# Kernel optimization log

Hardware: AMD Instinct MI355X
Metric: run time of the kernel (lower is better)

## Reference

```python
import jax, jax.numpy as jnp
import numpy as np

N, P, C, H, W, M = 2, 3, 80, 64, 64, 524288
HID = 64
BOX_WARP = 2.0


def _linear_init(key, fan_in, fan_out):
    # kaiming-uniform-ish; bias is zero-init per the torch module
    bound = 1.0 / np.sqrt(fan_in)
    return jax.random.uniform(key, (fan_in, fan_out), jnp.float32, -bound, bound)


def setup_inputs() -> dict:
    key = jax.random.key(0)
    ks = jax.random.split(key, 6)
    planes = jax.random.normal(ks[0], (N, P, C, H, W), jnp.float32)
    coordinates = jax.random.uniform(ks[1], (N, M, 3), jnp.float32, -1.0, 1.0)
    W1 = _linear_init(ks[2], 3 * C, HID)
    W2 = _linear_init(ks[3], HID, HID)
    W3 = _linear_init(ks[4], HID, HID)
    W4 = _linear_init(ks[5], HID, 1)
    return {
        "planes": planes, "coordinates": coordinates,
        "W1": W1, "b1": jnp.zeros((HID,), jnp.float32),
        "W2": W2, "b2": jnp.zeros((HID,), jnp.float32),
        "W3": W3, "b3": jnp.zeros((HID,), jnp.float32),
        "W4": W4, "b4": jnp.zeros((1,), jnp.float32),
    }


def _grid_sample_bilinear(feat, grid):
    # feat: [B, C, H, W]; grid: [B, M, 2] in [-1, 1] (x, y order),
    # bilinear, padding_mode='zeros', align_corners=False (matches torch).
    B, Cc, Hh, Ww = feat.shape
    gx = (grid[..., 0] + 1.0) * (Ww * 0.5) - 0.5  # [B, M]
    gy = (grid[..., 1] + 1.0) * (Hh * 0.5) - 0.5
    x0 = jnp.floor(gx)
    y0 = jnp.floor(gy)
    wx1 = gx - x0
    wy1 = gy - y0
    featf = feat.transpose(0, 2, 3, 1).reshape(B, Hh * Ww, Cc)  # [B, HW, C]

    def gather(xi, yi):
        valid = (xi >= 0) & (xi < Ww) & (yi >= 0) & (yi < Hh)
        xc = jnp.clip(xi, 0, Ww - 1).astype(jnp.int32)
        yc = jnp.clip(yi, 0, Hh - 1).astype(jnp.int32)
        idx = yc * Ww + xc  # [B, M]
        v = jnp.take_along_axis(featf, idx[..., None], axis=1)  # [B, M, C]
        return v * valid[..., None].astype(feat.dtype)

    v00 = gather(x0, y0)
    v01 = gather(x0 + 1, y0)
    v10 = gather(x0, y0 + 1)
    v11 = gather(x0 + 1, y0 + 1)
    wx1 = wx1[..., None]
    wy1 = wy1[..., None]
    top = v00 * (1.0 - wx1) + v01 * wx1
    bot = v10 * (1.0 - wx1) + v11 * wx1
    return top * (1.0 - wy1) + bot * wy1  # [B, M, C]


def _plane_axes():
    return jnp.array(
        [[[1, 0, 0], [0, 1, 0], [0, 0, 1]],
         [[1, 0, 0], [0, 0, 1], [0, 1, 0]],
         [[0, 0, 1], [0, 1, 0], [1, 0, 0]]], jnp.float32)


def reference(planes, coordinates, W1, b1, W2, b2, W3, b3, W4, b4):
    n, p, c, h, w = planes.shape
    m = coordinates.shape[1]
    inv_axes = jnp.linalg.inv(_plane_axes())  # [3, 3, 3]
    coords = (2.0 / BOX_WARP) * coordinates  # [N, M, 3]
    # project: coords @ inv_plane per plane, keep first two coords
    proj = jnp.einsum('nmc,pcd->npmd', coords, inv_axes)[..., :2]  # [N, P, M, 2]
    feat = planes.reshape(n * p, c, h, w)
    grid = proj.reshape(n * p, m, 2)
    samp = _grid_sample_bilinear(feat, grid)  # [N*P, M, C]
    # [N, P, M, C] -> [N, M, P*C]
    x = samp.reshape(n, p, m, c).transpose(0, 2, 1, 3).reshape(n, m, p * c)
    hdn = jax.nn.relu(x @ W1 + b1)
    hdn = jax.nn.relu(hdn @ W2 + b2)
    hdn = jax.nn.relu(hdn @ W3 + b3)
    sdf = hdn @ W4 + b4  # [N, M, 1]
    return sdf
```

## Files before the change

kernel.cpp:

```cpp
#include <hip/hip_runtime.h>
#include <hip/hip_bf16.h>
#include <stdint.h>

#define MPTS  524288
#define NB    2
#define CCH   80
#define HWDIM 64
#define HID   64
#define NPTS  (NB * MPTS)

typedef _Float16 f16x2 __attribute__((ext_vector_type(2)));
typedef _Float16 f16x8 __attribute__((ext_vector_type(8)));
typedef float    f32x4 __attribute__((ext_vector_type(4)));

union FragH { uint4 q; f16x8 v; f16x2 h2[4]; unsigned d[4]; _Float16 h[8]; };
union PkU   { f16x2 v; unsigned u; };

__device__ __forceinline__ void pk_fma(unsigned& acc, unsigned a, unsigned b) {
    asm volatile("v_pk_fma_f16 %0, %1, %2, %0" : "+v"(acc) : "v"(a), "v"(b));
}
__device__ __forceinline__ unsigned pk_relu(unsigned a) {
    unsigned r;
    asm volatile("v_pk_max_f16 %0, %1, %2" : "=v"(r) : "v"(a), "v"(0u));
    return r;
}

__global__ void precompute_planesW(const float* __restrict__ planes,
                                   const float* __restrict__ W1,
                                   unsigned short* __restrict__ planesW) {
    __shared__ float tA[CCH * 64];
    __shared__ float tW[CCH * 64];
    int b  = blockIdx.x;
    int np = b >> 6, y = b & 63;
    int p  = np % 3;
    int t  = threadIdx.x;
    for (int i = t; i < CCH * 64; i += 256) {
        int c = i >> 6, x = i & 63;
        tA[i] = planes[((size_t)np * CCH + c) * 4096 + y * 64 + x];
        tW[i] = W1[(p * CCH + c) * HID + x];
    }
    __syncthreads();
    int px = t >> 2;
    int n0 = (t & 3) * 16;
    float acc[16];
    #pragma unroll
    for (int i = 0; i < 16; ++i) acc[i] = 0.0f;
    for (int c = 0; c < CCH; ++c) {
        float a = tA[c * 64 + px];
        #pragma unroll
        for (int i = 0; i < 16; ++i) acc[i] += a * tW[c * 64 + n0 + i];
    }
    unsigned short* dst = planesW + (((size_t)np * 4096) + y * 64 + px) * HID + n0;
    #pragma unroll
    for (int i = 0; i < 16; ++i) {
        union { _Float16 h; unsigned short u; } cv;
        cv.h = (_Float16)acc[i];
        dst[i] = cv.u;
    }
}

__global__ void pack_weights23(const float* __restrict__ W2,
                               const float* __restrict__ W3,
                               unsigned short* __restrict__ wpack) {
    int e = blockIdx.x * 256 + threadIdx.x;
    const float* W = (e < 4096) ? W2 : W3;
    int q  = e & 4095;
    int j  = q & 7;
    int l  = (q >> 3) & 63;
    int nt = (q >> 9) & 3;
    int kb = q >> 11;
    int k  = kb * 32 + ((l >> 4) << 3) + j;
    int nn = nt * 16 + (l & 15);
    union { _Float16 h; unsigned short u; } cv;
    cv.h = (_Float16)W[k * HID + nn];
    wpack[e] = cv.u;
}

__global__ __launch_bounds__(512, 6) void fused_kernel(
        const unsigned short* __restrict__ planesW,
        const float* __restrict__ coords,
        const unsigned short* __restrict__ wpack,
        const float* __restrict__ b1, const float* __restrict__ b2,
        const float* __restrict__ b3, const float* __restrict__ W4,
        const float* __restrict__ b4, float* __restrict__ out) {

    __shared__ __align__(16) unsigned short sH[8 * 16 * 72];
    __shared__ __align__(16) uint4 sSet[128][3][2];
    __shared__ __align__(16) unsigned short sW23[8192];
    __shared__ float sBias[196];

    int t    = threadIdx.x;
    int wave = t >> 6, lane = t & 63;
    int ptbase = blockIdx.x * 128 + wave * 16;

    unsigned short* hw = sH + wave * (16 * 72);
    _Float16* hwh = (_Float16*)hw;

    {
        const uint4* g = (const uint4*)wpack;
        uint4* s = (uint4*)sW23;
        s[t]       = g[t];
        s[t + 512] = g[t + 512];
        if (t < 64)        sBias[t] = b2[t];
        else if (t < 128)  sBias[t] = b3[t - 64];
        else if (t < 192)  sBias[t] = W4[t - 128];
        else if (t == 192) sBias[192] = b4[0];
    }

    if (t < 384) {
        int i  = t & 127;
        int p  = t >> 7;
        int mypt = blockIdx.x * 128 + i;
        int n    = mypt >> 19;
        const float* cp = coords + (size_t)mypt * 3;
        float c0 = cp[0], c1 = cp[1], c2 = cp[2];
        float gx = (p == 2) ? c2 : c0;
        float gy = (p == 1) ? c2 : c1;
        float fx = (gx + 1.0f) * 32.0f - 0.5f;
        float fy = (gy + 1.0f) * 32.0f - 0.5f;
        float xf = floorf(fx), yf = floorf(fy);
        float wx = fx - xf,    wy = fy - yf;
        int x0 = (int)xf, y0 = (int)yf, x1 = x0 + 1, y1 = y0 + 1;
        float vx0 = (x0 >= 0 && x0 < 64) ? 1.0f : 0.0f;
        float vx1 = (x1 >= 0 && x1 < 64) ? 1.0f : 0.0f;
        float vy0 = (y0 >= 0 && y0 < 64) ? 1.0f : 0.0f;
        float vy1 = (y1 >= 0 && y1 < 64) ? 1.0f : 0.0f;
        int cx0 = min(max(x0, 0), 63), cx1 = min(max(x1, 0), 63);
        int cy0 = min(max(y0, 0), 63), cy1 = min(max(y1, 0), 63);
        float f00 = (1.0f - wx) * (1.0f - wy) * vx0 * vy0;
        float f01 = wx * (1.0f - wy) * vx1 * vy0;
        float f10 = (1.0f - wx) * wy * vx0 * vy1;
        float f11 = wx * wy * vx1 * vy1;
        uint4 wq;
        { PkU pk; _Float16 h;
          h = (_Float16)f00; pk.v = f16x2{h, h}; wq.x = pk.u;
          h = (_Float16)f01; pk.v = f16x2{h, h}; wq.y = pk.u;
          h = (_Float16)f10; pk.v = f16x2{h, h}; wq.z = pk.u;
          h = (_Float16)f11; pk.v = f16x2{h, h}; wq.w = pk.u; }
        int base = (n * 3 + p) * 4096;
        uint4 oq;
        oq.x = (unsigned)((base + (cy0 << 6) + cx0) * HID);
        oq.y = (unsigned)((base + (cy0 << 6) + cx1) * HID);
        oq.z = (unsigned)((base + (cy1 << 6) + cx0) * HID);
        oq.w = (unsigned)((base + (cy1 << 6) + cx1) * HID);
        sSet[i][p][0] = oq;
        sSet[i][p][1] = wq;
    }
    __syncthreads();

    {
        int sub = lane & 7;
        int ptg = lane >> 3;

        unsigned bp0, bp1, bp2, bp3;
        {
            const float4* bpp = (const float4*)(b1 + sub * 8);
            float4 v0 = bpp[0], v1 = bpp[1];
            PkU pk;
            pk.v = f16x2{(_Float16)v0.x, (_Float16)v0.y}; bp0 = pk.u;
            pk.v = f16x2{(_Float16)v0.z, (_Float16)v0.w}; bp1 = pk.u;
            pk.v = f16x2{(_Float16)v1.x, (_Float16)v1.y}; bp2 = pk.u;
            pk.v = f16x2{(_Float16)v1.z, (_Float16)v1.w}; bp3 = pk.u;
        }
        const unsigned short* pw = planesW + sub * 8;

        auto do_round = [&](int pt) {
            int pl = wave * 16 + pt;
            uint4 o0 = sSet[pl][0][0], w0c = sSet[pl][0][1];
            uint4 o1 = sSet[pl][1][0], w1c = sSet[pl][1][1];
            uint4 o2 = sSet[pl][2][0], w2c = sSet[pl][2][1];

            FragH u0, u1, u2, u3, u4, u5, u6, u7, u8, u9, u10, u11;
            u0.q  = *(const uint4*)(pw + o0.x);
            u1.q  = *(const uint4*)(pw + o0.y);
            u2.q  = *(const uint4*)(pw + o0.z);
            u3.q  = *(const uint4*)(pw + o0.w);
            u4.q  = *(const uint4*)(pw + o1.x);
            u5.q  = *(const uint4*)(pw + o1.y);
            u6.q  = *(const uint4*)(pw + o1.z);
            u7.q  = *(const uint4*)(pw + o1.w);
            u8.q  = *(const uint4*)(pw + o2.x);
            u9.q  = *(const uint4*)(pw + o2.y);
            u10.q = *(const uint4*)(pw + o2.z);
            u11.q = *(const uint4*)(pw + o2.w);

            unsigned a0 = bp0, a1 = bp1, a2 = bp2, a3 = bp3;

            #define TEXEL(T, WB) { pk_fma(a0, T.d[0], WB); pk_fma(a1, T.d[1], WB); \
                                   pk_fma(a2, T.d[2], WB); pk_fma(a3, T.d[3], WB); }
            TEXEL(u0,  w0c.x) TEXEL(u1,  w0c.y) TEXEL(u2,  w0c.z) TEXEL(u3,  w0c.w)
            TEXEL(u4,  w1c.x) TEXEL(u5,  w1c.y) TEXEL(u6,  w1c.z) TEXEL(u7,  w1c.w)
            TEXEL(u8,  w2c.x) TEXEL(u9,  w2c.y) TEXEL(u10, w2c.z) TEXEL(u11, w2c.w)
            #undef TEXEL

            uint4 hv;
            hv.x = pk_relu(a0); hv.y = pk_relu(a1);
            hv.z = pk_relu(a2); hv.w = pk_relu(a3);
            *(uint4*)(hwh + pt * 72 + sub * 8) = hv;
        };
        do_round(ptg);
        do_round(8 + ptg);
    }

    int row  = lane & 15;
    int kgrp = lane >> 4;
    f32x4 acc2[4] = {{0,0,0,0},{0,0,0,0},{0,0,0,0},{0,0,0,0}};
    #pragma unroll
    for (int kk = 0; kk < 2; ++kk) {
        FragH au;
        au.q = *(const uint4*)(hw + row * 72 + kk * 32 + kgrp * 8);
        #pragma unroll
        for (int nt = 0; nt < 4; ++nt) {
            FragH bu;
            bu.q = *(const uint4*)(sW23 + (kk * 4 + nt) * 512 + lane * 8);
            acc2[nt] = __builtin_amdgcn_mfma_f32_16x16x32_f16(au.v, bu.v, acc2[nt], 0, 0, 0);
        }
    }

    #pragma unroll
    for (int nt = 0; nt < 4; ++nt) {
        float bb = sBias[nt * 16 + row];
        #pragma unroll
        for (int r = 0; r < 4; ++r) {
            float h = fmaxf(acc2[nt][r] + bb, 0.0f);
            hwh[(kgrp * 4 + r) * 72 + nt * 16 + row] = (_Float16)h;
        }
    }

    f32x4 acc3[4] = {{0,0,0,0},{0,0,0,0},{0,0,0,0},{0,0,0,0}};
    #pragma unroll
    for (int kk = 0; kk < 2; ++kk) {
        FragH au;
        au.q = *(const uint4*)(hw + row * 72 + kk * 32 + kgrp * 8);
        #pragma unroll
        for (int nt = 0; nt < 4; ++nt) {
            FragH bu;
            bu.q = *(const uint4*)(sW23 + 4096 + (kk * 4 + nt) * 512 + lane * 8);
            acc3[nt] = __builtin_amdgcn_mfma_f32_16x16x32_f16(au.v, bu.v, acc3[nt], 0, 0, 0);
        }
    }

    float part[4] = {0.f, 0.f, 0.f, 0.f};
    #pragma unroll
    for (int nt = 0; nt < 4; ++nt) {
        float bb  = sBias[64 + nt * 16 + row];
        float w4v = sBias[128 + nt * 16 + row];
        #pragma unroll
        for (int r = 0; r < 4; ++r) {
            float h = fmaxf(acc3[nt][r] + bb, 0.0f);
            part[r] += h * w4v;
        }
    }
    #pragma unroll
    for (int r = 0; r < 4; ++r) {
        #pragma unroll
        for (int off = 1; off < 16; off <<= 1)
            part[r] += __shfl_xor(part[r], off);
    }
    if (row == 0) {
        float bias4 = sBias[192];
        float4 o;
        o.x = part[0] + bias4; o.y = part[1] + bias4;
        o.z = part[2] + bias4; o.w = part[3] + bias4;
        *(float4*)(out + ptbase + kgrp * 4) = o;
    }
}

extern "C" void kernel_launch(void* const* d_in, const int* in_sizes, int n_in,
                              void* d_out, int out_size, void* d_ws, size_t ws_size,
                              hipStream_t stream) {
    const float* planes = (const float*)d_in[0];
    const float* coords = (const float*)d_in[1];
    const float* W1 = (const float*)d_in[2];
    const float* b1 = (const float*)d_in[3];
    const float* W2 = (const float*)d_in[4];
    const float* b2 = (const float*)d_in[5];
    const float* W3 = (const float*)d_in[6];
    const float* b3 = (const float*)d_in[7];
    const float* W4 = (const float*)d_in[8];
    const float* b4 = (const float*)d_in[9];
    float* out = (float*)d_out;

    unsigned short* planesW = (unsigned short*)d_ws;
    unsigned short* wpack   = (unsigned short*)((char*)d_ws + 3145728);

    hipLaunchKernelGGL(precompute_planesW, dim3(NB * 3 * HWDIM), dim3(256), 0, stream,
                       planes, W1, planesW);
    hipLaunchKernelGGL(pack_weights23, dim3(32), dim3(256), 0, stream,
                       W2, W3, wpack);

    int nblocks = NPTS / 128;
    hipLaunchKernelGGL(fused_kernel, dim3(nblocks), dim3(512), 0, stream,
                       planesW, coords, wpack, b1, b2, b3, W4, b4, out);
}
```

Before: 90.53 us.

## Compute sampling setup per lane and defer weight staging past gather phase

Drops the shared-memory staging of per-point sampling offsets and weights along with the barrier before the gather. Each lane now recomputes the bilinear setup for its own point across the three planes, redundantly across the 8 channel-subgroup lanes. The W2/W3 and bias loads are issued into registers early and written to LDS after the gather, with a single barrier before the MFMA stage. Removing sSet lowers LDS use, and launch bounds rise to 8 blocks per CU, trading register pressure and extra ALU work for more occupancy and one fewer sync.

```diff
diff --git a/kernel.cpp b/kernel.cpp
--- a/kernel.cpp
+++ b/kernel.cpp
@@ -76,7 +76,7 @@
     wpack[e] = cv.u;
 }
 
-__global__ __launch_bounds__(512, 6) void fused_kernel(
+__global__ __launch_bounds__(512, 8) void fused_kernel(
         const unsigned short* __restrict__ planesW,
         const float* __restrict__ coords,
         const unsigned short* __restrict__ wpack,
@@ -85,9 +85,8 @@
         const float* __restrict__ b4, float* __restrict__ out) {
 
     __shared__ __align__(16) unsigned short sH[8 * 16 * 72];
-    __shared__ __align__(16) uint4 sSet[128][3][2];
     __shared__ __align__(16) unsigned short sW23[8192];
-    __shared__ float sBias[196];
+    __shared__ float sBias[200];
 
     int t    = threadIdx.x;
     int wave = t >> 6, lane = t & 63;
@@ -96,57 +95,17 @@
     unsigned short* hw = sH + wave * (16 * 72);
     _Float16* hwh = (_Float16*)hw;
 
+    uint4 st0, st1;
     {
         const uint4* g = (const uint4*)wpack;
-        uint4* s = (uint4*)sW23;
-        s[t]       = g[t];
-        s[t + 512] = g[t + 512];
-        if (t < 64)        sBias[t] = b2[t];
-        else if (t < 128)  sBias[t] = b3[t - 64];
-        else if (t < 192)  sBias[t] = W4[t - 128];
-        else if (t == 192) sBias[192] = b4[0];
-    }
-
-    if (t < 384) {
-        int i  = t & 127;
-        int p  = t >> 7;
-        int mypt = blockIdx.x * 128 + i;
-        int n    = mypt >> 19;
-        const float* cp = coords + (size_t)mypt * 3;
-        float c0 = cp[0], c1 = cp[1], c2 = cp[2];
-        float gx = (p == 2) ? c2 : c0;
-        float gy = (p == 1) ? c2 : c1;
-        float fx = (gx + 1.0f) * 32.0f - 0.5f;
-        float fy = (gy + 1.0f) * 32.0f - 0.5f;
-        float xf = floorf(fx), yf = floorf(fy);
-        float wx = fx - xf,    wy = fy - yf;
-        int x0 = (int)xf, y0 = (int)yf, x1 = x0 + 1, y1 = y0 + 1;
-        float vx0 = (x0 >= 0 && x0 < 64) ? 1.0f : 0.0f;
-        float vx1 = (x1 >= 0 && x1 < 64) ? 1.0f : 0.0f;
-        float vy0 = (y0 >= 0 && y0 < 64) ? 1.0f : 0.0f;
-        float vy1 = (y1 >= 0 && y1 < 64) ? 1.0f : 0.0f;
-        int cx0 = min(max(x0, 0), 63), cx1 = min(max(x1, 0), 63);
-        int cy0 = min(max(y0, 0), 63), cy1 = min(max(y1, 0), 63);
-        float f00 = (1.0f - wx) * (1.0f - wy) * vx0 * vy0;
-        float f01 = wx * (1.0f - wy) * vx1 * vy0;
-        float f10 = (1.0f - wx) * wy * vx0 * vy1;
-        float f11 = wx * wy * vx1 * vy1;
-        uint4 wq;
-        { PkU pk; _Float16 h;
-          h = (_Float16)f00; pk.v = f16x2{h, h}; wq.x = pk.u;
-          h = (_Float16)f01; pk.v = f16x2{h, h}; wq.y = pk.u;
-          h = (_Float16)f10; pk.v = f16x2{h, h}; wq.z = pk.u;
-          h = (_Float16)f11; pk.v = f16x2{h, h}; wq.w = pk.u; }
-        int base = (n * 3 + p) * 4096;
-        uint4 oq;
-        oq.x = (unsigned)((base + (cy0 << 6) + cx0) * HID);
-        oq.y = (unsigned)((base + (cy0 << 6) + cx1) * HID);
-        oq.z = (unsigned)((base + (cy1 << 6) + cx0) * HID);
-        oq.w = (unsigned)((base + (cy1 << 6) + cx1) * HID);
-        sSet[i][p][0] = oq;
-        sSet[i][p][1] = wq;
-    }
-    __syncthreads();
+        st0 = g[t];
+        st1 = g[t + 512];
+    }
+    float br = 0.0f;
+    if (t < 64)        br = b2[t];
+    else if (t < 128)  br = b3[t - 64];
+    else if (t < 192)  br = W4[t - 128];
+    else if (t == 192) br = b4[0];
 
     {
         int sub = lane & 7;
@@ -164,33 +123,67 @@
         }
         const unsigned short* pw = planesW + sub * 8;
 
+        #define SETUP(GX, GY, PBASE, OA, OB, OC, OD, WA, WB, WC, WD)              \
+        {   float fx = ((GX) + 1.0f) * 32.0f - 0.5f;                              \
+            float fy = ((GY) + 1.0f) * 32.0f - 0.5f;                              \
+            float xf = floorf(fx), yf = floorf(fy);                               \
+            float wx = fx - xf,    wy = fy - yf;                                  \
+            int x0 = (int)xf, y0 = (int)yf, x1 = x0 + 1, y1 = y0 + 1;             \
+            float vx0 = (x0 >= 0 && x0 < 64) ? 1.0f : 0.0f;                       \
+            float vx1 = (x1 >= 0 && x1 < 64) ? 1.0f : 0.0f;                       \
+            float vy0 = (y0 >= 0 && y0 < 64) ? 1.0f : 0.0f;                       \
+            float vy1 = (y1 >= 0 && y1 < 64) ? 1.0f : 0.0f;                       \
+            int cx0 = min(max(x0, 0), 63), cx1 = min(max(x1, 0), 63);             \
+            int cy0 = min(max(y0, 0), 63), cy1 = min(max(y1, 0), 63);             \
+            PkU pk; _Float16 hh;                                                  \
+            hh = (_Float16)((1.0f - wx) * (1.0f - wy) * vx0 * vy0);               \
+            pk.v = f16x2{hh, hh}; WA = pk.u;                                      \
+            hh = (_Float16)(wx * (1.0f - wy) * vx1 * vy0);                        \
+            pk.v = f16x2{hh, hh}; WB = pk.u;                                      \
+            hh = (_Float16)((1.0f - wx) * wy * vx0 * vy1);                        \
+            pk.v = f16x2{hh, hh}; WC = pk.u;                                      \
+            hh = (_Float16)(wx * wy * vx1 * vy1);                                 \
+            pk.v = f16x2{hh, hh}; WD = pk.u;                                      \
+            OA = (unsigned)(((PBASE) + (cy0 << 6) + cx0) * HID);                  \
+            OB = (unsigned)(((PBASE) + (cy0 << 6) + cx1) * HID);                  \
+            OC = (unsigned)(((PBASE) + (cy1 << 6) + cx0) * HID);                  \
+            OD = (unsigned)(((PBASE) + (cy1 << 6) + cx1) * HID); }
+
         auto do_round = [&](int pt) {
-            int pl = wave * 16 + pt;
-            uint4 o0 = sSet[pl][0][0], w0c = sSet[pl][0][1];
-            uint4 o1 = sSet[pl][1][0], w1c = sSet[pl][1][1];
-            uint4 o2 = sSet[pl][2][0], w2c = sSet[pl][2][1];
+            int mypt = ptbase + pt;
+            int n    = mypt >> 19;
+            const float* cp = coords + (size_t)mypt * 3;
+            float c0 = cp[0], c1 = cp[1], c2 = cp[2];
+            int base0 = n * 3 * 4096;
+
+            unsigned oA0, oA1, oA2, oA3, wA0, wA1, wA2, wA3;
+            unsigned oB0, oB1, oB2, oB3, wB0, wB1, wB2, wB3;
+            unsigned oC0, oC1, oC2, oC3, wC0, wC1, wC2, wC3;
+            SETUP(c0, c1, base0,        oA0, oA1, oA2, oA3, wA0, wA1, wA2, wA3)
+            SETUP(c0, c2, base0 + 4096, oB0, oB1, oB2, oB3, wB0, wB1, wB2, wB3)
+            SETUP(c2, c1, base0 + 8192, oC0, oC1, oC2, oC3, wC0, wC1, wC2, wC3)
 
             FragH u0, u1, u2, u3, u4, u5, u6, u7, u8, u9, u10, u11;
-            u0.q  = *(const uint4*)(pw + o0.x);
-            u1.q  = *(const uint4*)(pw + o0.y);
-            u2.q  = *(const uint4*)(pw + o0.z);
-            u3.q  = *(const uint4*)(pw + o0.w);
-            u4.q  = *(const uint4*)(pw + o1.x);
-            u5.q  = *(const uint4*)(pw + o1.y);
-            u6.q  = *(const uint4*)(pw + o1.z);
-            u7.q  = *(const uint4*)(pw + o1.w);
-            u8.q  = *(const uint4*)(pw + o2.x);
-            u9.q  = *(const uint4*)(pw + o2.y);
-            u10.q = *(const uint4*)(pw + o2.z);
-            u11.q = *(const uint4*)(pw + o2.w);
+            u0.q  = *(const uint4*)(pw + oA0);
+            u1.q  = *(const uint4*)(pw + oA1);
+            u2.q  = *(const uint4*)(pw + oA2);
+            u3.q  = *(const uint4*)(pw + oA3);
+            u4.q  = *(const uint4*)(pw + oB0);
+            u5.q  = *(const uint4*)(pw + oB1);
+            u6.q  = *(const uint4*)(pw + oB2);
+            u7.q  = *(const uint4*)(pw + oB3);
+            u8.q  = *(const uint4*)(pw + oC0);
+            u9.q  = *(const uint4*)(pw + oC1);
+            u10.q = *(const uint4*)(pw + oC2);
+            u11.q = *(const uint4*)(pw + oC3);
 
             unsigned a0 = bp0, a1 = bp1, a2 = bp2, a3 = bp3;
 
-            #define TEXEL(T, WB) { pk_fma(a0, T.d[0], WB); pk_fma(a1, T.d[1], WB); \
-                                   pk_fma(a2, T.d[2], WB); pk_fma(a3, T.d[3], WB); }
-            TEXEL(u0,  w0c.x) TEXEL(u1,  w0c.y) TEXEL(u2,  w0c.z) TEXEL(u3,  w0c.w)
-            TEXEL(u4,  w1c.x) TEXEL(u5,  w1c.y) TEXEL(u6,  w1c.z) TEXEL(u7,  w1c.w)
-            TEXEL(u8,  w2c.x) TEXEL(u9,  w2c.y) TEXEL(u10, w2c.z) TEXEL(u11, w2c.w)
+            #define TEXEL(T, WB_) { pk_fma(a0, T.d[0], WB_); pk_fma(a1, T.d[1], WB_); \
+                                    pk_fma(a2, T.d[2], WB_); pk_fma(a3, T.d[3], WB_); }
+            TEXEL(u0,  wA0) TEXEL(u1,  wA1) TEXEL(u2,  wA2) TEXEL(u3,  wA3)
+            TEXEL(u4,  wB0) TEXEL(u5,  wB1) TEXEL(u6,  wB2) TEXEL(u7,  wB3)
+            TEXEL(u8,  wC0) TEXEL(u9,  wC1) TEXEL(u10, wC2) TEXEL(u11, wC3)
             #undef TEXEL
 
             uint4 hv;
@@ -200,7 +193,16 @@
         };
         do_round(ptg);
         do_round(8 + ptg);
-    }
+        #undef SETUP
+    }
+
+    {
+        uint4* s = (uint4*)sW23;
+        s[t]       = st0;
+        s[t + 512] = st1;
+        if (t <= 192) sBias[t] = br;
+    }
+    __syncthreads();
 
     int row  = lane & 15;
     int kgrp = lane >> 4;
```

After: 204.0 us. 125% more time.
